# Optimization experiments

Measured on AMD Instinct MI355X. Metric: run time of the kernel, lower is better.

Reference implementation:

```python
import jax, jax.numpy as jnp
import numpy as np
import math

O0, O1 = 64, 64
I0, I1 = 128, 128
B = 32


def setup_inputs() -> dict:
    key = jax.random.key(0)
    kx, kw, kb = jax.random.split(key, 3)
    x = jax.random.normal(kx, (B, I0, I1), dtype=jnp.float32)
    # kaiming_uniform_(a=sqrt(5)) on weight of shape [O0,O1,I0,I1]:
    # fan_in = I0 * I1; gain = sqrt(2/(1+a^2)) = sqrt(1/3); bound = gain*sqrt(3/fan_in) = 1/sqrt(fan_in)
    fan_in = I0 * I1
    wbound = 1.0 / math.sqrt(fan_in)
    weight = jax.random.uniform(kw, (O0, O1, I0, I1), minval=-wbound, maxval=wbound, dtype=jnp.float32)
    bbound = 1.0 / math.sqrt(fan_in)
    bias = jax.random.uniform(kb, (O0, O1), minval=-bbound, maxval=bbound, dtype=jnp.float32)
    return {"x": x, "weight": weight, "bias": bias}


def reference(x, weight, bias):
    # Original torch code computes W^T @ x -> [O0,O1,B,I1,I1], takes the diagonal
    # over the last two dims and sums: out[b,p,o] = sum_{i,j} W[p,o,i,j] * x[b,i,j].
    # Direct contraction avoids materializing the off-diagonal entries.
    out = jnp.einsum('poij,bij->bpo', weight, x) + bias  # [B, O0, O1]
    return out
```

## Files before the change

### kernel.cpp

```cpp
#include <hip/hip_runtime.h>


typedef __attribute__((ext_vector_type(8))) __bf16 bf16x8;
typedef __attribute__((ext_vector_type(4))) __bf16 bf16x4;
typedef __attribute__((ext_vector_type(4))) float f32x4;

#define KDIM 16384
#define NPO  4096
#define POT  32
#define CHK  256
#define KH   8192
#define NCHH 32
#define WSTR 264

__device__ inline bf16x8 cvt8(float4 a, float4 b) {
  bf16x8 r;
  r[0] = (__bf16)a.x; r[1] = (__bf16)a.y; r[2] = (__bf16)a.z; r[3] = (__bf16)a.w;
  r[4] = (__bf16)b.x; r[5] = (__bf16)b.y; r[6] = (__bf16)b.z; r[7] = (__bf16)b.w;
  return r;
}

__global__ __launch_bounds__(256)
void precast_x(const float* __restrict__ x, __bf16* __restrict__ xbf) {
  const int i = blockIdx.x * 256 + threadIdx.x;
  float4 v = reinterpret_cast<const float4*>(x)[i];
  bf16x4 o;
  o[0] = (__bf16)v.x; o[1] = (__bf16)v.y; o[2] = (__bf16)v.z; o[3] = (__bf16)v.w;
  reinterpret_cast<bf16x4*>(xbf)[i] = o;
}

__global__ __launch_bounds__(512, 2)
void trace_main(const __bf16* __restrict__ xbf, const float* __restrict__ w,
                float* __restrict__ part) {
  __shared__ __bf16 wbuf[2][32 * WSTR];
  __shared__ __bf16 xbuf[2][32 * WSTR];
  __shared__ float  red[2048];

  const int t    = threadIdx.x;
  const int lane = t & 63;
  const int wv   = t >> 6;
  const int btile  = wv & 1;
  const int potile = (wv >> 1) & 1;
  const int kq     = wv >> 2;
  const int kh    = blockIdx.x & 1;
  const int group = blockIdx.x >> 1;
  const int po_base = group * POT;

  const int row_s = t >> 4;
  const int col_s = (t & 15) * 16;
  const float*  wg = w   + (size_t)(po_base + row_s) * KDIM + (size_t)kh * KH + col_s;
  const __bf16* xg = xbf + (size_t)row_s * KDIM + (size_t)kh * KH + col_s;
  const int soff = row_s * WSTR + col_s;

  const int lrow = lane & 15, lhi = lane >> 4;
  const int fk  = kq * 128 + lhi * 8;
  const int wfo = (potile * 16 + lrow) * WSTR + fk;
  const int xfo = (btile * 16 + lrow) * WSTR + fk;

  f32x4 acc = {0.f, 0.f, 0.f, 0.f};

#define ISSUE(W4, X2, c) do {                              \
    const float*  wp_ = wg + (size_t)(c) * CHK;            \
    const __bf16* xp_ = xg + (size_t)(c) * CHK;            \
    W4[0] = *(const float4*)(wp_);                         \
    W4[1] = *(const float4*)(wp_ + 4);                     \
    W4[2] = *(const float4*)(wp_ + 8);                     \
    W4[3] = *(const float4*)(wp_ + 12);                    \
    X2[0] = *(const bf16x8*)(xp_);                         \
    X2[1] = *(const bf16x8*)(xp_ + 8);                     \
  } while (0)

#define WRITE_LDS(W4, X2, h) do {                          \
    *(bf16x8*)&wbuf[h][soff]     = cvt8(W4[0], W4[1]);     \
    *(bf16x8*)&wbuf[h][soff + 8] = cvt8(W4[2], W4[3]);     \
    *(bf16x8*)&xbuf[h][soff]     = X2[0];                  \
    *(bf16x8*)&xbuf[h][soff + 8] = X2[1];                  \
  } while (0)

#define COMPUTE(h) do {                                    \
    _Pragma("unroll")                                      \
    for (int j = 0; j < 4; ++j) {                          \
      bf16x8 bf_ = *(const bf16x8*)&wbuf[h][wfo + j * 32]; \
      bf16x8 af_ = *(const bf16x8*)&xbuf[h][xfo + j * 32]; \
      acc = __builtin_amdgcn_mfma_f32_16x16x32_bf16(af_, bf_, acc, 0, 0, 0); \
    }                                                      \
  } while (0)

#define BARRIER() do {                                     \
    asm volatile("s_waitcnt lgkmcnt(0)" ::: "memory");     \
    __builtin_amdgcn_s_barrier();                          \
  } while (0)

  float4 raw[4], rbw[4];
  bf16x8 rax[2], rbx[2];

  ISSUE(raw, rax, 0);
  WRITE_LDS(raw, rax, 0);
  ISSUE(raw, rax, 1);
  BARRIER();

  for (int c = 0; c < NCHH; c += 2) {
    if (c + 2 < NCHH) ISSUE(rbw, rbx, c + 2);
    COMPUTE(0);
    WRITE_LDS(raw, rax, 1);
    BARRIER();
    if (c + 3 < NCHH) ISSUE(raw, rax, c + 3);
    COMPUTE(1);
    if (c + 2 < NCHH) WRITE_LDS(rbw, rbx, 0);
    BARRIER();
  }

#undef ISSUE
#undef WRITE_LDS
#undef COMPUTE
#undef BARRIER

  red[wv * 256 + lane * 4 + 0] = acc[0];
  red[wv * 256 + lane * 4 + 1] = acc[1];
  red[wv * 256 + lane * 4 + 2] = acc[2];
  red[wv * 256 + lane * 4 + 3] = acc[3];
  __syncthreads();

#pragma unroll
  for (int i0 = 0; i0 < 2; ++i0) {
    const int i    = i0 * 512 + t;
    const int tile = i >> 8;
    const int slot = i & 255;
    const float v = red[tile * 256 + slot] + red[(tile + 4) * 256 + slot];
    const int ln = slot >> 2, rg = slot & 3;
    const int b  = (tile & 1) * 16 + (ln >> 4) * 4 + rg;
    const int pl = (tile >> 1) * 16 + (ln & 15);
    part[((size_t)(kh * 128 + group) * 32 + b) * 32 + pl] = v;
  }
}

__global__ __launch_bounds__(256)
void combine(const float* __restrict__ part, const float* __restrict__ bias,
             float* __restrict__ out) {
  const int i = blockIdx.x * 256 + threadIdx.x;
  const int pl = i & 31, b = (i >> 5) & 31, g = i >> 10;
  const float v = part[i] + part[131072 + i] + bias[g * 32 + pl];
  out[(size_t)b * NPO + g * 32 + pl] = v;
}

extern "C" void kernel_launch(void* const* d_in, const int* in_sizes, int n_in,
                              void* d_out, int out_size, void* d_ws, size_t ws_size,
                              hipStream_t stream) {
  const float* x    = (const float*)d_in[0];
  const float* wgt  = (const float*)d_in[1];
  const float* bias = (const float*)d_in[2];
  float* out = (float*)d_out;

  __bf16* xbf = (__bf16*)d_ws;
  float*  part = (float*)((char*)d_ws + (1 << 20));

  hipLaunchKernelGGL(precast_x, dim3(512), dim3(256), 0, stream, x, xbf);
  hipLaunchKernelGGL(trace_main, dim3(256), dim3(512), 0, stream, xbf, wgt, part);
  hipLaunchKernelGGL(combine, dim3(512), dim3(256), 0, stream, part, bias, out);
}
```

Before: 56.12 us.

## Widen output tile to 64 rows and split K four ways across blocks

Each block now covers 64 output (p,o) rows instead of 32, so every staged x chunk is reused across twice as many weight rows. The K dimension is split into four quarters across blocks instead of two, and each warp owns a whole 16x16 tile over the full chunk K. This removes the in-block LDS reduction and its barrier. In exchange the weight LDS buffer doubles, more register staging is needed per thread, and the combine kernel now sums four partial buffers.

```diff
diff --git a/kernel.cpp b/kernel.cpp
--- a/kernel.cpp
+++ b/kernel.cpp
@@ -7,10 +7,10 @@
 
 #define KDIM 16384
 #define NPO  4096
-#define POT  32
+#define POT  64
 #define CHK  256
-#define KH   8192
-#define NCHH 32
+#define KQTR 4096
+#define NCHH 16
 #define WSTR 264
 
 __device__ inline bf16x8 cvt8(float4 a, float4 b) {
@@ -32,56 +32,55 @@
 __global__ __launch_bounds__(512, 2)
 void trace_main(const __bf16* __restrict__ xbf, const float* __restrict__ w,
                 float* __restrict__ part) {
-  __shared__ __bf16 wbuf[2][32 * WSTR];
+  __shared__ __bf16 wbuf[2][64 * WSTR];
   __shared__ __bf16 xbuf[2][32 * WSTR];
-  __shared__ float  red[2048];
 
   const int t    = threadIdx.x;
   const int lane = t & 63;
   const int wv   = t >> 6;
   const int btile  = wv & 1;
-  const int potile = (wv >> 1) & 1;
-  const int kq     = wv >> 2;
-  const int kh    = blockIdx.x & 1;
-  const int group = blockIdx.x >> 1;
+  const int potile = wv >> 1;
+  const int kh    = blockIdx.x & 3;
+  const int group = blockIdx.x >> 2;
   const int po_base = group * POT;
 
-  const int row_s = t >> 4;
-  const int col_s = (t & 15) * 16;
-  const float*  wg = w   + (size_t)(po_base + row_s) * KDIM + (size_t)kh * KH + col_s;
-  const __bf16* xg = xbf + (size_t)row_s * KDIM + (size_t)kh * KH + col_s;
-  const int soff = row_s * WSTR + col_s;
+  const int wrow_s = t >> 3, wcol_s = (t & 7) * 32;
+  const int xrow_s = t >> 4, xcol_s = (t & 15) * 16;
+  const float*  wg = w   + (size_t)(po_base + wrow_s) * KDIM + (size_t)kh * KQTR + wcol_s;
+  const __bf16* xg = xbf + (size_t)xrow_s * KDIM + (size_t)kh * KQTR + xcol_s;
+  const int woff = wrow_s * WSTR + wcol_s;
+  const int xoff = xrow_s * WSTR + xcol_s;
 
   const int lrow = lane & 15, lhi = lane >> 4;
-  const int fk  = kq * 128 + lhi * 8;
-  const int wfo = (potile * 16 + lrow) * WSTR + fk;
-  const int xfo = (btile * 16 + lrow) * WSTR + fk;
+  const int wfo = (potile * 16 + lrow) * WSTR + lhi * 8;
+  const int xfo = (btile * 16 + lrow) * WSTR + lhi * 8;
 
   f32x4 acc = {0.f, 0.f, 0.f, 0.f};
 
-#define ISSUE(W4, X2, c) do {                              \
+#define ISSUE(W8, X2, c) do {                              \
     const float*  wp_ = wg + (size_t)(c) * CHK;            \
     const __bf16* xp_ = xg + (size_t)(c) * CHK;            \
-    W4[0] = *(const float4*)(wp_);                         \
-    W4[1] = *(const float4*)(wp_ + 4);                     \
-    W4[2] = *(const float4*)(wp_ + 8);                     \
-    W4[3] = *(const float4*)(wp_ + 12);                    \
+    _Pragma("unroll")                                      \
+    for (int j_ = 0; j_ < 8; ++j_)                         \
+      W8[j_] = *(const float4*)(wp_ + j_ * 4);             \
     X2[0] = *(const bf16x8*)(xp_);                         \
     X2[1] = *(const bf16x8*)(xp_ + 8);                     \
   } while (0)
 
-#define WRITE_LDS(W4, X2, h) do {                          \
-    *(bf16x8*)&wbuf[h][soff]     = cvt8(W4[0], W4[1]);     \
-    *(bf16x8*)&wbuf[h][soff + 8] = cvt8(W4[2], W4[3]);     \
-    *(bf16x8*)&xbuf[h][soff]     = X2[0];                  \
-    *(bf16x8*)&xbuf[h][soff + 8] = X2[1];                  \
+#define WRITE_LDS(W8, X2, h) do {                          \
+    *(bf16x8*)&wbuf[h][woff]      = cvt8(W8[0], W8[1]);    \
+    *(bf16x8*)&wbuf[h][woff + 8]  = cvt8(W8[2], W8[3]);    \
+    *(bf16x8*)&wbuf[h][woff + 16] = cvt8(W8[4], W8[5]);    \
+    *(bf16x8*)&wbuf[h][woff + 24] = cvt8(W8[6], W8[7]);    \
+    *(bf16x8*)&xbuf[h][xoff]      = X2[0];                 \
+    *(bf16x8*)&xbuf[h][xoff + 8]  = X2[1];                 \
   } while (0)
 
 #define COMPUTE(h) do {                                    \
     _Pragma("unroll")                                      \
-    for (int j = 0; j < 4; ++j) {                          \
-      bf16x8 bf_ = *(const bf16x8*)&wbuf[h][wfo + j * 32]; \
-      bf16x8 af_ = *(const bf16x8*)&xbuf[h][xfo + j * 32]; \
+    for (int j_ = 0; j_ < 8; ++j_) {                       \
+      bf16x8 bf_ = *(const bf16x8*)&wbuf[h][wfo + j_ * 32];\
+      bf16x8 af_ = *(const bf16x8*)&xbuf[h][xfo + j_ * 32];\
       acc = __builtin_amdgcn_mfma_f32_16x16x32_bf16(af_, bf_, acc, 0, 0, 0); \
     }                                                      \
   } while (0)
@@ -91,7 +90,7 @@
     __builtin_amdgcn_s_barrier();                          \
   } while (0)
 
-  float4 raw[4], rbw[4];
+  float4 raw[8], rbw[8];
   bf16x8 rax[2], rbx[2];
 
   ISSUE(raw, rax, 0);
@@ -115,32 +114,21 @@
 #undef COMPUTE
 #undef BARRIER
 
-  red[wv * 256 + lane * 4 + 0] = acc[0];
-  red[wv * 256 + lane * 4 + 1] = acc[1];
-  red[wv * 256 + lane * 4 + 2] = acc[2];
-  red[wv * 256 + lane * 4 + 3] = acc[3];
-  __syncthreads();
-
+  const int b  = btile * 16 + lhi * 4;
+  const int pl = potile * 16 + lrow;
 #pragma unroll
-  for (int i0 = 0; i0 < 2; ++i0) {
-    const int i    = i0 * 512 + t;
-    const int tile = i >> 8;
-    const int slot = i & 255;
-    const float v = red[tile * 256 + slot] + red[(tile + 4) * 256 + slot];
-    const int ln = slot >> 2, rg = slot & 3;
-    const int b  = (tile & 1) * 16 + (ln >> 4) * 4 + rg;
-    const int pl = (tile >> 1) * 16 + (ln & 15);
-    part[((size_t)(kh * 128 + group) * 32 + b) * 32 + pl] = v;
-  }
+  for (int r = 0; r < 4; ++r)
+    part[(((size_t)kh * 64 + group) * 32 + (b + r)) * 64 + pl] = acc[r];
 }
 
 __global__ __launch_bounds__(256)
 void combine(const float* __restrict__ part, const float* __restrict__ bias,
              float* __restrict__ out) {
   const int i = blockIdx.x * 256 + threadIdx.x;
-  const int pl = i & 31, b = (i >> 5) & 31, g = i >> 10;
-  const float v = part[i] + part[131072 + i] + bias[g * 32 + pl];
-  out[(size_t)b * NPO + g * 32 + pl] = v;
+  const int pl = i & 63, b = (i >> 6) & 31, g = i >> 11;
+  const float v = part[i] + part[131072 + i] + part[262144 + i] + part[393216 + i]
+                + bias[g * 64 + pl];
+  out[(size_t)b * NPO + g * 64 + pl] = v;
 }
 
 extern "C" void kernel_launch(void* const* d_in, const int* in_sizes, int n_in,
@@ -151,7 +139,7 @@
   const float* bias = (const float*)d_in[2];
   float* out = (float*)d_out;
 
-  __bf16* xbf = (__bf16*)d_ws;
+  __bf16* xbf  = (__bf16*)d_ws;
   float*  part = (float*)((char*)d_ws + (1 << 20));
 
   hipLaunchKernelGGL(precast_x, dim3(512), dim3(256), 0, stream, x, xbf);
```

Result: slower. 64.55 us (+15.0%).

## Halve output tile per block, fuse x cast into main kernel, drop precast

Applied to the files above, without the earlier changes.

Each block now covers 16 outputs instead of 32, which doubles the grid to 512 blocks, and launch bounds ask for 4 blocks per CU. The separate x precast kernel is removed: each block reads fp32 x and converts it to bf16 while writing LDS. This removes one kernel launch and spreads the weight stream over more blocks, in exchange for every block re-reading and converting x, which doubles the x traffic and conversion work across the grid.

```diff
diff --git a/kernel.cpp b/kernel.cpp
--- a/kernel.cpp
+++ b/kernel.cpp
@@ -2,12 +2,11 @@
 
 
 typedef __attribute__((ext_vector_type(8))) __bf16 bf16x8;
-typedef __attribute__((ext_vector_type(4))) __bf16 bf16x4;
 typedef __attribute__((ext_vector_type(4))) float f32x4;
 
 #define KDIM 16384
 #define NPO  4096
-#define POT  32
+#define POT  16
 #define CHK  256
 #define KH   8192
 #define NCHH 32
@@ -20,68 +19,58 @@
   return r;
 }
 
-__global__ __launch_bounds__(256)
-void precast_x(const float* __restrict__ x, __bf16* __restrict__ xbf) {
-  const int i = blockIdx.x * 256 + threadIdx.x;
-  float4 v = reinterpret_cast<const float4*>(x)[i];
-  bf16x4 o;
-  o[0] = (__bf16)v.x; o[1] = (__bf16)v.y; o[2] = (__bf16)v.z; o[3] = (__bf16)v.w;
-  reinterpret_cast<bf16x4*>(xbf)[i] = o;
-}
-
-__global__ __launch_bounds__(512, 2)
-void trace_main(const __bf16* __restrict__ xbf, const float* __restrict__ w,
+__global__ __launch_bounds__(512, 4)
+void trace_main(const float* __restrict__ x, const float* __restrict__ w,
                 float* __restrict__ part) {
-  __shared__ __bf16 wbuf[2][32 * WSTR];
+  __shared__ __bf16 wbuf[2][16 * WSTR];
   __shared__ __bf16 xbuf[2][32 * WSTR];
   __shared__ float  red[2048];
 
   const int t    = threadIdx.x;
   const int lane = t & 63;
   const int wv   = t >> 6;
-  const int btile  = wv & 1;
-  const int potile = (wv >> 1) & 1;
-  const int kq     = wv >> 2;
+  const int btile = wv & 1;
+  const int kq    = wv >> 1;
   const int kh    = blockIdx.x & 1;
   const int group = blockIdx.x >> 1;
   const int po_base = group * POT;
 
-  const int row_s = t >> 4;
-  const int col_s = (t & 15) * 16;
-  const float*  wg = w   + (size_t)(po_base + row_s) * KDIM + (size_t)kh * KH + col_s;
-  const __bf16* xg = xbf + (size_t)row_s * KDIM + (size_t)kh * KH + col_s;
-  const int soff = row_s * WSTR + col_s;
+  const int wrow_s = t >> 5, wcol_s = (t & 31) * 8;
+  const int xrow_s = t >> 4, xcol_s = (t & 15) * 16;
+  const float* wg = w + (size_t)(po_base + wrow_s) * KDIM + (size_t)kh * KH + wcol_s;
+  const float* xg = x + (size_t)xrow_s * KDIM + (size_t)kh * KH + xcol_s;
+  const int woff = wrow_s * WSTR + wcol_s;
+  const int xoff = xrow_s * WSTR + xcol_s;
 
   const int lrow = lane & 15, lhi = lane >> 4;
-  const int fk  = kq * 128 + lhi * 8;
-  const int wfo = (potile * 16 + lrow) * WSTR + fk;
+  const int fk  = kq * 64 + lhi * 8;
+  const int wfo = lrow * WSTR + fk;
   const int xfo = (btile * 16 + lrow) * WSTR + fk;
 
   f32x4 acc = {0.f, 0.f, 0.f, 0.f};
 
-#define ISSUE(W4, X2, c) do {                              \
-    const float*  wp_ = wg + (size_t)(c) * CHK;            \
-    const __bf16* xp_ = xg + (size_t)(c) * CHK;            \
-    W4[0] = *(const float4*)(wp_);                         \
-    W4[1] = *(const float4*)(wp_ + 4);                     \
-    W4[2] = *(const float4*)(wp_ + 8);                     \
-    W4[3] = *(const float4*)(wp_ + 12);                    \
-    X2[0] = *(const bf16x8*)(xp_);                         \
-    X2[1] = *(const bf16x8*)(xp_ + 8);                     \
+#define ISSUE(W2, X4, c) do {                              \
+    const float* wp_ = wg + (size_t)(c) * CHK;             \
+    const float* xp_ = xg + (size_t)(c) * CHK;             \
+    W2[0] = *(const float4*)(wp_);                         \
+    W2[1] = *(const float4*)(wp_ + 4);                     \
+    X4[0] = *(const float4*)(xp_);                         \
+    X4[1] = *(const float4*)(xp_ + 4);                     \
+    X4[2] = *(const float4*)(xp_ + 8);                     \
+    X4[3] = *(const float4*)(xp_ + 12);                    \
   } while (0)
 
-#define WRITE_LDS(W4, X2, h) do {                          \
-    *(bf16x8*)&wbuf[h][soff]     = cvt8(W4[0], W4[1]);     \
-    *(bf16x8*)&wbuf[h][soff + 8] = cvt8(W4[2], W4[3]);     \
-    *(bf16x8*)&xbuf[h][soff]     = X2[0];                  \
-    *(bf16x8*)&xbuf[h][soff + 8] = X2[1];                  \
+#define WRITE_LDS(W2, X4, h) do {                          \
+    *(bf16x8*)&wbuf[h][woff]     = cvt8(W2[0], W2[1]);     \
+    *(bf16x8*)&xbuf[h][xoff]     = cvt8(X4[0], X4[1]);     \
+    *(bf16x8*)&xbuf[h][xoff + 8] = cvt8(X4[2], X4[3]);     \
   } while (0)
 
 #define COMPUTE(h) do {                                    \
     _Pragma("unroll")                                      \
-    for (int j = 0; j < 4; ++j) {                          \
-      bf16x8 bf_ = *(const bf16x8*)&wbuf[h][wfo + j * 32]; \
-      bf16x8 af_ = *(const bf16x8*)&xbuf[h][xfo + j * 32]; \
+    for (int j_ = 0; j_ < 2; ++j_) {                       \
+      bf16x8 bf_ = *(const bf16x8*)&wbuf[h][wfo + j_ * 32];\
+      bf16x8 af_ = *(const bf16x8*)&xbuf[h][xfo + j_ * 32];\
       acc = __builtin_amdgcn_mfma_f32_16x16x32_bf16(af_, bf_, acc, 0, 0, 0); \
     }                                                      \
   } while (0)
@@ -91,8 +80,8 @@
     __builtin_amdgcn_s_barrier();                          \
   } while (0)
 
-  float4 raw[4], rbw[4];
-  bf16x8 rax[2], rbx[2];
+  float4 raw[2], rbw[2];
+  float4 rax[4], rbx[4];
 
   ISSUE(raw, rax, 0);
   WRITE_LDS(raw, rax, 0);
@@ -121,26 +110,23 @@
   red[wv * 256 + lane * 4 + 3] = acc[3];
   __syncthreads();
 
-#pragma unroll
-  for (int i0 = 0; i0 < 2; ++i0) {
-    const int i    = i0 * 512 + t;
-    const int tile = i >> 8;
-    const int slot = i & 255;
-    const float v = red[tile * 256 + slot] + red[(tile + 4) * 256 + slot];
-    const int ln = slot >> 2, rg = slot & 3;
-    const int b  = (tile & 1) * 16 + (ln >> 4) * 4 + rg;
-    const int pl = (tile >> 1) * 16 + (ln & 15);
-    part[((size_t)(kh * 128 + group) * 32 + b) * 32 + pl] = v;
-  }
+  const int bt2  = t >> 8;
+  const int slot = t & 255;
+  const float v = red[bt2 * 256 + slot]       + red[bt2 * 256 + slot + 512]
+                + red[bt2 * 256 + slot + 1024] + red[bt2 * 256 + slot + 1536];
+  const int ln = slot >> 2, rg = slot & 3;
+  const int b  = bt2 * 16 + (ln >> 4) * 4 + rg;
+  const int pl = ln & 15;
+  part[((size_t)(kh * 256 + group) * 32 + b) * 16 + pl] = v;
 }
 
 __global__ __launch_bounds__(256)
 void combine(const float* __restrict__ part, const float* __restrict__ bias,
              float* __restrict__ out) {
   const int i = blockIdx.x * 256 + threadIdx.x;
-  const int pl = i & 31, b = (i >> 5) & 31, g = i >> 10;
-  const float v = part[i] + part[131072 + i] + bias[g * 32 + pl];
-  out[(size_t)b * NPO + g * 32 + pl] = v;
+  const int pl = i & 15, b = (i >> 4) & 31, g = i >> 9;
+  const float v = part[i] + part[131072 + i] + bias[g * 16 + pl];
+  out[(size_t)b * NPO + g * 16 + pl] = v;
 }
 
 extern "C" void kernel_launch(void* const* d_in, const int* in_sizes, int n_in,
@@ -151,10 +137,8 @@
   const float* bias = (const float*)d_in[2];
   float* out = (float*)d_out;
 
-  __bf16* xbf = (__bf16*)d_ws;
-  float*  part = (float*)((char*)d_ws + (1 << 20));
+  float* part = (float*)d_ws;
 
-  hipLaunchKernelGGL(precast_x, dim3(512), dim3(256), 0, stream, x, xbf);
-  hipLaunchKernelGGL(trace_main, dim3(256), dim3(512), 0, stream, xbf, wgt, part);
+  hipLaunchKernelGGL(trace_main, dim3(512), dim3(512), 0, stream, x, wgt, part);
   hipLaunchKernelGGL(combine, dim3(512), dim3(256), 0, stream, part, bias, out);
 }
```

Result: slower. 64.62 us (+15.2%).
